# Performance work log

Measured on AMD Instinct MI355X. Metric: run time of the kernel, lower is better.

Reference implementation:

```python
import jax, jax.numpy as jnp
import numpy as np

T, B, D = 512, 32, 1024

def setup_inputs() -> dict:
    key = jax.random.key(0)
    ks = jax.random.split(key, 4)
    scale = 1.0 / np.sqrt(D)
    x = jax.random.normal(ks[0], (T, B, D), dtype=jnp.float32)
    h0 = jnp.zeros((B, D), dtype=jnp.float32)
    W_alpha = jax.random.normal(ks[1], (D, D), dtype=jnp.float32) * scale
    b_alpha = jnp.zeros((D,), dtype=jnp.float32)
    # W_h in torch is orthogonal * 0.3; approximate with scaled gaussian of matching norm
    W_h = jax.random.normal(ks[2], (D, D), dtype=jnp.float32) * (0.3 * scale)
    W_x = jax.random.normal(ks[3], (D, D), dtype=jnp.float32) * scale
    b = jnp.zeros((D,), dtype=jnp.float32)
    return {"x": x, "h0": h0, "W_alpha": W_alpha, "b_alpha": b_alpha,
            "W_h": W_h, "W_x": W_x, "b": b}

def reference(x, h0, W_alpha, b_alpha, W_h, W_x, b):
    # Precompute input-dependent projections for all timesteps (batched GEMM)
    alpha_x_all = jnp.einsum('tbd,ed->tbe', x, W_alpha) + b_alpha  # [T,B,D]
    Wx_all = jnp.einsum('tbd,ed->tbe', x, W_x)                     # [T,B,D]

    def step(h_prev, inp):
        alpha_x_t, wx_t = inp
        alpha = jax.nn.sigmoid(alpha_x_t)
        v = jnp.tanh(h_prev @ W_h.T + wx_t + b)
        h_new = h_prev + alpha * v  # residual: identity path always present
        return h_new, h_new

    _, h_seq = jax.lax.scan(step, h0, (alpha_x_all, Wx_all))  # [T,B,D]
    h = jnp.concatenate([h0[None], h_seq], axis=0)            # [T+1,B,D]
    output = h_seq * jax.nn.silu(h_seq)                       # h * silu(h)
    return output, h
```

## Files before the change

### kernel.cpp

```cpp
#include <hip/hip_runtime.h>

typedef __bf16 bf16x8 __attribute__((ext_vector_type(8)));
typedef float  f32x4  __attribute__((ext_vector_type(4)));
typedef unsigned short u16;
typedef unsigned int   u32;
typedef unsigned long long u64;
typedef u16 u16x8 __attribute__((ext_vector_type(8)));

#define TT 512
#define BB 32
#define DD 1024

#define WS_Z   0
#define WS_HX  134217728
#define WS_FLG (134217728+262144)

static __device__ __forceinline__ u16 f2b(float f){
  u32 u = __builtin_bit_cast(u32, f);
  u32 r = (u + 0x7fffu + ((u>>16)&1u)) >> 16;
  return (u16)r;
}
static __device__ __forceinline__ float b2f(u16 h){
  return __builtin_bit_cast(float, (u32)h<<16);
}

#define AL64(p)   __hip_atomic_load((p),      __ATOMIC_RELAXED, __HIP_MEMORY_SCOPE_AGENT)
#define AS32(p,v) __hip_atomic_store((p),(v), __ATOMIC_RELAXED, __HIP_MEMORY_SCOPE_AGENT)

#define MFMA16(a,b,c) __builtin_amdgcn_mfma_f32_16x16x32_bf16(a,b,c,0,0,0)

__global__ __launch_bounds__(256) void k_gemm3(const float* __restrict__ X,
    const float* __restrict__ Wa, const float* __restrict__ Wx,
    float* __restrict__ Z){
  __shared__ u16 Ahi[128*64];
  __shared__ u16 Alo[128*64];
  __shared__ u16 Bhi[128*64];
  __shared__ u16 Blo[128*64];
  int id  = blockIdx.x;
  int swz = (id & 7)*256 + (id>>3);
  int mblk = swz>>4, nblk = swz&15;
  const float* W = (nblk < 8) ? Wa : Wx;
  int n0 = (nblk&7)*128;
  int m0 = mblk*128;
  int tid = threadIdx.x, lane = tid&63, w = tid>>6;
  int wm = w>>1, wn = w&1;
  int sr = tid>>1, sh = tid&1;

  f32x4 acc[4][4];
  #pragma unroll
  for (int i=0;i<4;i++)
    #pragma unroll
    for (int j=0;j<4;j++) acc[i][j] = (f32x4){0.f,0.f,0.f,0.f};

  for (int kb = 0; kb < DD; kb += 64){
    const float* sa  = X + (size_t)(m0+sr)*DD + kb + sh*32;
    const float* sbp = W + (size_t)(n0+sr)*DD + kb + sh*32;
    int rswz = (sr&7)<<4;
    #pragma unroll
    for (int g=0; g<4; g++){
      float4 va0 = ((const float4*)sa)[g*2];
      float4 va1 = ((const float4*)sa)[g*2+1];
      float4 vb0 = ((const float4*)sbp)[g*2];
      float4 vb1 = ((const float4*)sbp)[g*2+1];
      float fa[8] = {va0.x,va0.y,va0.z,va0.w,va1.x,va1.y,va1.z,va1.w};
      float fb[8] = {vb0.x,vb0.y,vb0.z,vb0.w,vb1.x,vb1.y,vb1.z,vb1.w};
      u16x8 ah, al, bh, bl;
      #pragma unroll
      for (int j=0;j<8;j++){
        u16 ha = f2b(fa[j]); ah[j] = ha; al[j] = f2b(fa[j] - b2f(ha));
        u16 hb = f2b(fb[j]); bh[j] = hb; bl[j] = f2b(fb[j] - b2f(hb));
      }
      int off = sr*128 + ((sh*64 + g*16) ^ rswz);
      *(u16x8*)((char*)Ahi + off) = ah;
      *(u16x8*)((char*)Alo + off) = al;
      *(u16x8*)((char*)Bhi + off) = bh;
      *(u16x8*)((char*)Blo + off) = bl;
    }
    __syncthreads();
    #pragma unroll
    for (int ks=0; ks<2; ks++){
      int kby = ks*64 + ((lane>>4)<<4);
      bf16x8 ahf[4], alf[4], bhf[4], blf[4];
      #pragma unroll
      for (int mi=0;mi<4;mi++){
        int row = wm*64 + mi*16 + (lane&15);
        int ao = row*128 + (kby ^ ((row&7)<<4));
        ahf[mi] = *(const bf16x8*)((const char*)Ahi + ao);
        alf[mi] = *(const bf16x8*)((const char*)Alo + ao);
      }
      #pragma unroll
      for (int ni=0;ni<4;ni++){
        int row = wn*64 + ni*16 + (lane&15);
        int bo = row*128 + (kby ^ ((row&7)<<4));
        bhf[ni] = *(const bf16x8*)((const char*)Bhi + bo);
        blf[ni] = *(const bf16x8*)((const char*)Blo + bo);
      }
      #pragma unroll
      for (int mi=0;mi<4;mi++)
        #pragma unroll
        for (int ni=0;ni<4;ni++){
          acc[mi][ni] = MFMA16(ahf[mi], bhf[ni], acc[mi][ni]);
          acc[mi][ni] = MFMA16(ahf[mi], blf[ni], acc[mi][ni]);
          acc[mi][ni] = MFMA16(alf[mi], bhf[ni], acc[mi][ni]);
        }
    }
    __syncthreads();
  }

  #pragma unroll
  for (int mi=0;mi<4;mi++){
    #pragma unroll
    for (int ni=0;ni<4;ni++){
      int colz = nblk*128 + wn*64 + ni*16 + (lane&15);
      #pragma unroll
      for (int q=0;q<4;q++){
        int rowm = m0 + wm*64 + mi*16 + ((lane>>4)<<2) + q;
        Z[(size_t)rowm*2048 + colz] = acc[mi][ni][q];
      }
    }
  }
}

__global__ void k_init(const float* __restrict__ h0, float* __restrict__ hout0,
                       u32* __restrict__ hx, u32* __restrict__ flg){
  int i = blockIdx.x*blockDim.x + threadIdx.x;
  if (i < BB*DD){
    float v = h0[i];
    hout0[i] = v;
    u16 hh = f2b(v);
    u16 ll = f2b(v - b2f(hh));
    hx[i] = (u32)hh | ((u32)ll<<16);
  }
  if (i < 32) flg[i] = 0u;
}

#define UNPK(c, A, B) do { \
  u16x8 hi8, lo8; \
  hi8[0]=(u16)A.x; lo8[0]=(u16)(A.x>>16); \
  hi8[1]=(u16)A.y; lo8[1]=(u16)(A.y>>16); \
  hi8[2]=(u16)A.z; lo8[2]=(u16)(A.z>>16); \
  hi8[3]=(u16)A.w; lo8[3]=(u16)(A.w>>16); \
  hi8[4]=(u16)B.x; lo8[4]=(u16)(B.x>>16); \
  hi8[5]=(u16)B.y; lo8[5]=(u16)(B.y>>16); \
  hi8[6]=(u16)B.z; lo8[6]=(u16)(B.z>>16); \
  hi8[7]=(u16)B.w; lo8[7]=(u16)(B.w>>16); \
  int off_ = srow*2048 + ((kseg*128 + (c)*16) ^ ssw); \
  *(u16x8*)((char*)Hhi + off_) = hi8; \
  *(u16x8*)((char*)Hlo + off_) = lo8; \
} while(0)

__global__ __launch_bounds__(512, 2) void k_recur5(
    const float* __restrict__ Z, const float* __restrict__ Wh,
    const float* __restrict__ h0,
    const float* __restrict__ balpha, const float* __restrict__ bvec,
    float* __restrict__ out0,
    float* __restrict__ hout,
    u32* __restrict__ hx,
    u32* __restrict__ flg){
  __shared__ u16 Hhi[BB*DD];
  __shared__ u16 Hlo[BB*DD];
  __shared__ f32x4 Red[4][64];

  int blk = blockIdx.x, e0 = blk*32;
  int tid = threadIdx.x, lane = tid&63, w = tid>>6;
  int kh = w>>2, wm = (w>>1)&1, wn = w&1;

  bf16x8 wfh[16], wfl[16];
  {
    const float* wrow = Wh + (size_t)(e0 + wn*16 + (lane&15))*DD
                           + kh*512 + ((lane>>4)<<3);
    #pragma unroll
    for (int ks=0; ks<16; ks++){
      float4 a = ((const float4*)(wrow + ks*32))[0];
      float4 b = ((const float4*)(wrow + ks*32))[1];
      float f[8] = {a.x,a.y,a.z,a.w,b.x,b.y,b.z,b.w};
      u16x8 uh, ul;
      #pragma unroll
      for (int j=0;j<8;j++){
        u16 hh = f2b(f[j]);
        uh[j] = hh;
        ul[j] = f2b(f[j] - b2f(hh));
      }
      wfh[ks] = __builtin_bit_cast(bf16x8, uh);
      wfl[ks] = __builtin_bit_cast(bf16x8, ul);
    }
  }

  int el = e0 + wn*16 + (lane&15);
  float ba = balpha[el], bb = bvec[el];
  float hc[4]  = {0.f,0.f,0.f,0.f};
  float ov[4]  = {0.f,0.f,0.f,0.f};
  float axr[4] = {0.f,0.f,0.f,0.f};
  float wxr[4] = {0.f,0.f,0.f,0.f};
  if (kh == 0){
    #pragma unroll
    for (int q=0;q<4;q++){
      int b = wm*16 + ((lane>>4)<<2) + q;
      hc[q]  = h0[b*DD + el];
      axr[q] = Z[(size_t)b*2048 + el];
      wxr[q] = Z[(size_t)b*2048 + DD + el];
    }
  }

  int srow = tid & 31;
  int kseg = tid >> 5;
  int ssw  = (srow & 15) << 4;

  for (int t=0;t<TT;t++){
    if (tid < 16){
      const u64* fp = (const u64*)(flg + tid*2);
      u64 fl = AL64(fp);
      while ((u32)fl < (u32)t || (u32)(fl>>32) < (u32)t) fl = AL64(fp);
    }
    __syncthreads();

    const u32* hsrc = hx + (size_t)(t&1)*BB*DD;
    const void* gp = (const void*)(hsrc + srow*DD + kseg*64);
    uint4 r0,r1,r2,r3,r4,r5,r6,r7,r8,r9,rA,rB,rC,rD,rE,rF;
    asm volatile(
      "global_load_dwordx4 %0, %16, off sc1\n\t"
      "global_load_dwordx4 %1, %16, off offset:16 sc1\n\t"
      "global_load_dwordx4 %2, %16, off offset:32 sc1\n\t"
      "global_load_dwordx4 %3, %16, off offset:48 sc1\n\t"
      "global_load_dwordx4 %4, %16, off offset:64 sc1\n\t"
      "global_load_dwordx4 %5, %16, off offset:80 sc1\n\t"
      "global_load_dwordx4 %6, %16, off offset:96 sc1\n\t"
      "global_load_dwordx4 %7, %16, off offset:112 sc1\n\t"
      "global_load_dwordx4 %8, %16, off offset:128 sc1\n\t"
      "global_load_dwordx4 %9, %16, off offset:144 sc1\n\t"
      "global_load_dwordx4 %10, %16, off offset:160 sc1\n\t"
      "global_load_dwordx4 %11, %16, off offset:176 sc1\n\t"
      "global_load_dwordx4 %12, %16, off offset:192 sc1\n\t"
      "global_load_dwordx4 %13, %16, off offset:208 sc1\n\t"
      "global_load_dwordx4 %14, %16, off offset:224 sc1\n\t"
      "global_load_dwordx4 %15, %16, off offset:240 sc1\n\t"
      "s_waitcnt vmcnt(0)"
      : "=&v"(r0), "=&v"(r1), "=&v"(r2), "=&v"(r3),
        "=&v"(r4), "=&v"(r5), "=&v"(r6), "=&v"(r7),
        "=&v"(r8), "=&v"(r9), "=&v"(rA), "=&v"(rB),
        "=&v"(rC), "=&v"(rD), "=&v"(rE), "=&v"(rF)
      : "v"(gp)
      : "memory");
    UNPK(0, r0, r1);  UNPK(1, r2, r3);
    UNPK(2, r4, r5);  UNPK(3, r6, r7);
    UNPK(4, r8, r9);  UNPK(5, rA, rB);
    UNPK(6, rC, rD);  UNPK(7, rE, rF);

    float axc[4], wxc[4];
    if (kh == 0){
      #pragma unroll
      for (int q=0;q<4;q++){ axc[q]=axr[q]; wxc[q]=wxr[q]; }
      if (t < TT-1){
        #pragma unroll
        for (int q=0;q<4;q++){
          int b = wm*16 + ((lane>>4)<<2) + q;
          size_t zi = ((size_t)(t+1)*BB + b)*2048 + el;
          axr[q] = Z[zi]; wxr[q] = Z[zi + DD];
        }
      }
    } else {
      #pragma unroll
      for (int q=0;q<4;q++){ axc[q]=0.f; wxc[q]=0.f; }
    }
    __syncthreads();

    f32x4 a0 = (f32x4){0.f,0.f,0.f,0.f};
    f32x4 a1 = (f32x4){0.f,0.f,0.f,0.f};
    f32x4 a2 = (f32x4){0.f,0.f,0.f,0.f};
    int ra    = wm*16 + (lane&15);
    int rbase = ra*2048;
    int rsw   = (ra&15)<<4;
    int kb0   = kh*1024 + ((lane>>4)<<4);
    #pragma unroll
    for (int ks=0; ks<16; ks++){
      int off = rbase + ((kb0 + ks*64) ^ rsw);
      bf16x8 ahi = *(const bf16x8*)((const char*)Hhi + off);
      bf16x8 alo = *(const bf16x8*)((const char*)Hlo + off);
      a0 = MFMA16(ahi, wfh[ks], a0);
      a1 = MFMA16(ahi, wfl[ks], a1);
      a2 = MFMA16(alo, wfh[ks], a2);
    }
    f32x4 acc = a0 + a1 + a2;
    if (kh == 1){ Red[wm*2+wn][lane] = acc; }
    __syncthreads();

    if (kh == 0){
      acc += Red[wm*2+wn][lane];
      u32* hnx = hx + (size_t)((t+1)&1)*BB*DD;
      #pragma unroll
      for (int q=0;q<4;q++){
        int b = wm*16 + ((lane>>4)<<2) + q;
        float ax = axc[q] + ba;
        float alpha = 1.f/(1.f + __expf(-ax));
        float s  = acc[q] + wxc[q] + bb;
        float as = fabsf(s);
        float e2 = __expf(-2.f*as);
        float vv = __builtin_copysignf((1.f - e2)/(1.f + e2), s);
        float h = hc[q] + alpha*vv;
        hc[q] = h;
        float sg = 1.f/(1.f + __expf(-h));
        ov[q] = h*h*sg;
        u16 hh = f2b(h);
        u16 ll = f2b(h - b2f(hh));
        AS32(hnx + b*DD + el, (u32)hh | ((u32)ll<<16));
      }
    }

    __syncthreads();
    if (tid == 0) AS32(flg + blk, (u32)(t+1));

    if (kh == 0){
      #pragma unroll
      for (int q=0;q<4;q++){
        int b = wm*16 + ((lane>>4)<<2) + q;
        size_t oi = (size_t)t*(BB*DD) + (size_t)b*DD + el;
        out0[oi] = ov[q];
        hout[oi + BB*DD] = hc[q];
      }
    }
  }
}

extern "C" void kernel_launch(void* const* d_in, const int* in_sizes, int n_in,
                              void* d_out, int out_size, void* d_ws, size_t ws_size,
                              hipStream_t stream){
  (void)in_sizes; (void)n_in; (void)out_size; (void)ws_size;
  const float* x   = (const float*)d_in[0];
  const float* h0  = (const float*)d_in[1];
  const float* Wa  = (const float*)d_in[2];
  const float* bal = (const float*)d_in[3];
  const float* Whf = (const float*)d_in[4];
  const float* Wxf = (const float*)d_in[5];
  const float* bv  = (const float*)d_in[6];

  char* ws = (char*)d_ws;
  float* Zb  = (float*)(ws + WS_Z);
  u32*   hx  = (u32*)(ws + WS_HX);
  u32*   flg = (u32*)(ws + WS_FLG);

  float* out0 = (float*)d_out;
  float* hout = (float*)d_out + (size_t)TT*BB*DD;

  k_gemm3<<<2048, 256, 0, stream>>>(x, Wa, Wxf, Zb);
  k_init<<<(BB*DD+255)/256, 256, 0, stream>>>(h0, hout, hx, flg);

  void* args[] = {(void*)&Zb, (void*)&Whf, (void*)&h0, (void*)&bal, (void*)&bv,
                  (void*)&out0, (void*)&hout, (void*)&hx, (void*)&flg};
  hipLaunchCooperativeKernel((const void*)k_recur5, dim3(32), dim3(512),
                             args, 0, stream);
}
```

Measured before the change: 4.856 ms.

## Use per-wave completion flags and move Z prefetch after output stores

Each block used to publish one progress flag after a block-wide barrier. Now each of the four epilogue waves publishes its own flag right after its h stores drain, which removes the trailing __syncthreads. Consumers poll 128 flags using a whole wave of 64-bit loads. The next step's Z prefetch now runs after the output stores instead of in the critical load phase. This is meant to cut barrier and signaling latency in the serial recurrence, at the cost of more flag polling traffic.

```diff
diff --git a/kernel.cpp b/kernel.cpp
--- a/kernel.cpp
+++ b/kernel.cpp
@@ -131,7 +131,7 @@
     u16 ll = f2b(v - b2f(hh));
     hx[i] = (u32)hh | ((u32)ll<<16);
   }
-  if (i < 32) flg[i] = 0u;
+  if (i < 128) flg[i] = 0u;
 }
 
 #define UNPK(c, A, B) do { \
@@ -149,7 +149,40 @@
   *(u16x8*)((char*)Hlo + off_) = lo8; \
 } while(0)
 
-__global__ __launch_bounds__(512, 2) void k_recur5(
+#define BURST16(SC) \
+    asm volatile( \
+      "global_load_dwordx4 %0, %16, off " SC "\n\t" \
+      "global_load_dwordx4 %1, %16, off offset:16 " SC "\n\t" \
+      "global_load_dwordx4 %2, %16, off offset:32 " SC "\n\t" \
+      "global_load_dwordx4 %3, %16, off offset:48 " SC "\n\t" \
+      "global_load_dwordx4 %4, %16, off offset:64 " SC "\n\t" \
+      "global_load_dwordx4 %5, %16, off offset:80 " SC "\n\t" \
+      "global_load_dwordx4 %6, %16, off offset:96 " SC "\n\t" \
+      "global_load_dwordx4 %7, %16, off offset:112 " SC "\n\t" \
+      "global_load_dwordx4 %8, %16, off offset:128 " SC "\n\t" \
+      "global_load_dwordx4 %9, %16, off offset:144 " SC "\n\t" \
+      "global_load_dwordx4 %10, %16, off offset:160 " SC "\n\t" \
+      "global_load_dwordx4 %11, %16, off offset:176 " SC "\n\t" \
+      "global_load_dwordx4 %12, %16, off offset:192 " SC "\n\t" \
+      "global_load_dwordx4 %13, %16, off offset:208 " SC "\n\t" \
+      "global_load_dwordx4 %14, %16, off offset:224 " SC "\n\t" \
+      "global_load_dwordx4 %15, %16, off offset:240 " SC "\n\t" \
+      "s_waitcnt vmcnt(0)" \
+      : "=&v"(r0), "=&v"(r1), "=&v"(r2), "=&v"(r3), \
+        "=&v"(r4), "=&v"(r5), "=&v"(r6), "=&v"(r7), \
+        "=&v"(r8), "=&v"(r9), "=&v"(rA), "=&v"(rB), \
+        "=&v"(rC), "=&v"(rD), "=&v"(rE), "=&v"(rF) \
+      : "v"(gp) \
+      : "memory")
+
+#define UNPK_ALL() do { \
+    UNPK(0, r0, r1);  UNPK(1, r2, r3); \
+    UNPK(2, r4, r5);  UNPK(3, r6, r7); \
+    UNPK(4, r8, r9);  UNPK(5, rA, rB); \
+    UNPK(6, rC, rD);  UNPK(7, rE, rF); \
+} while(0)
+
+__global__ __launch_bounds__(512, 2) void k_recur8(
     const float* __restrict__ Z, const float* __restrict__ Wh,
     const float* __restrict__ h0,
     const float* __restrict__ balpha, const float* __restrict__ bvec,
@@ -189,7 +222,6 @@
   int el = e0 + wn*16 + (lane&15);
   float ba = balpha[el], bb = bvec[el];
   float hc[4]  = {0.f,0.f,0.f,0.f};
-  float ov[4]  = {0.f,0.f,0.f,0.f};
   float axr[4] = {0.f,0.f,0.f,0.f};
   float wxr[4] = {0.f,0.f,0.f,0.f};
   if (kh == 0){
@@ -207,8 +239,8 @@
   int ssw  = (srow & 15) << 4;
 
   for (int t=0;t<TT;t++){
-    if (tid < 16){
-      const u64* fp = (const u64*)(flg + tid*2);
+    if (w == 4){
+      const u64* fp = (const u64*)flg + lane;
       u64 fl = AL64(fp);
       while ((u32)fl < (u32)t || (u32)(fl>>32) < (u32)t) fl = AL64(fp);
     }
@@ -217,51 +249,8 @@
     const u32* hsrc = hx + (size_t)(t&1)*BB*DD;
     const void* gp = (const void*)(hsrc + srow*DD + kseg*64);
     uint4 r0,r1,r2,r3,r4,r5,r6,r7,r8,r9,rA,rB,rC,rD,rE,rF;
-    asm volatile(
-      "global_load_dwordx4 %0, %16, off sc1\n\t"
-      "global_load_dwordx4 %1, %16, off offset:16 sc1\n\t"
-      "global_load_dwordx4 %2, %16, off offset:32 sc1\n\t"
-      "global_load_dwordx4 %3, %16, off offset:48 sc1\n\t"
-      "global_load_dwordx4 %4, %16, off offset:64 sc1\n\t"
-      "global_load_dwordx4 %5, %16, off offset:80 sc1\n\t"
-      "global_load_dwordx4 %6, %16, off offset:96 sc1\n\t"
-      "global_load_dwordx4 %7, %16, off offset:112 sc1\n\t"
-      "global_load_dwordx4 %8, %16, off offset:128 sc1\n\t"
-      "global_load_dwordx4 %9, %16, off offset:144 sc1\n\t"
-      "global_load_dwordx4 %10, %16, off offset:160 sc1\n\t"
-      "global_load_dwordx4 %11, %16, off offset:176 sc1\n\t"
-      "global_load_dwordx4 %12, %16, off offset:192 sc1\n\t"
-      "global_load_dwordx4 %13, %16, off offset:208 sc1\n\t"
-      "global_load_dwordx4 %14, %16, off offset:224 sc1\n\t"
-      "global_load_dwordx4 %15, %16, off offset:240 sc1\n\t"
-      "s_waitcnt vmcnt(0)"
-      : "=&v"(r0), "=&v"(r1), "=&v"(r2), "=&v"(r3),
-        "=&v"(r4), "=&v"(r5), "=&v"(r6), "=&v"(r7),
-        "=&v"(r8), "=&v"(r9), "=&v"(rA), "=&v"(rB),
-        "=&v"(rC), "=&v"(rD), "=&v"(rE), "=&v"(rF)
-      : "v"(gp)
-      : "memory");
-    UNPK(0, r0, r1);  UNPK(1, r2, r3);
-    UNPK(2, r4, r5);  UNPK(3, r6, r7);
-    UNPK(4, r8, r9);  UNPK(5, rA, rB);
-    UNPK(6, rC, rD);  UNPK(7, rE, rF);
-
-    float axc[4], wxc[4];
-    if (kh == 0){
-      #pragma unroll
-      for (int q=0;q<4;q++){ axc[q]=axr[q]; wxc[q]=wxr[q]; }
-      if (t < TT-1){
-        #pragma unroll
-        for (int q=0;q<4;q++){
-          int b = wm*16 + ((lane>>4)<<2) + q;
-          size_t zi = ((size_t)(t+1)*BB + b)*2048 + el;
-          axr[q] = Z[zi]; wxr[q] = Z[zi + DD];
-        }
-      }
-    } else {
-      #pragma unroll
-      for (int q=0;q<4;q++){ axc[q]=0.f; wxc[q]=0.f; }
-    }
+    BURST16("sc1");
+    UNPK_ALL();
     __syncthreads();
 
     f32x4 a0 = (f32x4){0.f,0.f,0.f,0.f};
@@ -287,12 +276,13 @@
     if (kh == 0){
       acc += Red[wm*2+wn][lane];
       u32* hnx = hx + (size_t)((t+1)&1)*BB*DD;
+      float ov[4];
       #pragma unroll
       for (int q=0;q<4;q++){
         int b = wm*16 + ((lane>>4)<<2) + q;
-        float ax = axc[q] + ba;
+        float ax = axr[q] + ba;
         float alpha = 1.f/(1.f + __expf(-ax));
-        float s  = acc[q] + wxc[q] + bb;
+        float s  = acc[q] + wxr[q] + bb;
         float as = fabsf(s);
         float e2 = __expf(-2.f*as);
         float vv = __builtin_copysignf((1.f - e2)/(1.f + e2), s);
@@ -304,18 +294,22 @@
         u16 ll = f2b(h - b2f(hh));
         AS32(hnx + b*DD + el, (u32)hh | ((u32)ll<<16));
       }
-    }
-
-    __syncthreads();
-    if (tid == 0) AS32(flg + blk, (u32)(t+1));
-
-    if (kh == 0){
+      asm volatile("s_waitcnt vmcnt(0)" ::: "memory");
+      if (lane == 0) AS32(flg + blk*4 + w, (u32)(t+1));
       #pragma unroll
       for (int q=0;q<4;q++){
         int b = wm*16 + ((lane>>4)<<2) + q;
         size_t oi = (size_t)t*(BB*DD) + (size_t)b*DD + el;
         out0[oi] = ov[q];
         hout[oi + BB*DD] = hc[q];
+      }
+      if (t < TT-1){
+        #pragma unroll
+        for (int q=0;q<4;q++){
+          int b = wm*16 + ((lane>>4)<<2) + q;
+          size_t zi = ((size_t)(t+1)*BB + b)*2048 + el;
+          axr[q] = Z[zi]; wxr[q] = Z[zi + DD];
+        }
       }
     }
   }
@@ -346,6 +340,6 @@
 
   void* args[] = {(void*)&Zb, (void*)&Whf, (void*)&h0, (void*)&bal, (void*)&bv,
                   (void*)&out0, (void*)&hout, (void*)&hx, (void*)&flg};
-  hipLaunchCooperativeKernel((const void*)k_recur5, dim3(32), dim3(512),
+  hipLaunchCooperativeKernel((const void*)k_recur8, dim3(32), dim3(512),
                              args, 0, stream);
 }
```

Result: slower. 5.534 ms (+14.0%).
